# Kernel optimization log

Measured on AMD Instinct MI355X. Metric: run time of the kernel, lower is better.

## Reference

```python
import jax, jax.numpy as jnp
import numpy as np

N = 100000   # nodes
E = 1600000  # edges
D_IN = 128
H = 64
L = 3        # num SAGE layers
G = 512      # graphs in batch


def setup_inputs() -> dict:
    key = jax.random.key(0)
    ks = jax.random.split(key, 12)
    s = 0.05
    return {
        "x": jax.random.normal(ks[0], (N, D_IN), dtype=jnp.float32),
        "edge_index": jax.random.randint(ks[1], (2, E), 0, N, dtype=jnp.int64),
        "edge_attr": jax.random.normal(ks[2], (E, 1), dtype=jnp.float32),
        "batch": jnp.sort(jax.random.randint(ks[3], (N,), 0, G, dtype=jnp.int64)),
        "W0": jax.random.normal(ks[4], (D_IN, H), dtype=jnp.float32) * s,
        "b0": jnp.zeros((H,), dtype=jnp.float32),
        "Wl": jax.random.normal(ks[5], (L, H, H), dtype=jnp.float32) * s,  # lin_l (aggregated neighbors), has bias
        "bl": jnp.zeros((L, H), dtype=jnp.float32),
        "Wr": jax.random.normal(ks[6], (L, H, H), dtype=jnp.float32) * s,  # lin_r (root), no bias
        "W1": jax.random.normal(ks[7], (H, H), dtype=jnp.float32) * s,
        "b1": jnp.zeros((H,), dtype=jnp.float32),
    }


def reference(x, edge_index, edge_attr, batch, W0, b0, Wl, bl, Wr, W1, b1):
    # edge_attr is accepted but unused, matching the torch module.
    h = jax.nn.relu(x @ W0 + b0)                    # [N, H]
    src, dst = edge_index[0], edge_index[1]
    ones_e = jnp.ones((E,), dtype=h.dtype)
    deg = jax.ops.segment_sum(ones_e, dst, num_segments=N)
    deg = jnp.clip(deg, 1.0)[:, None]               # avoid div by zero (PyG mean -> 0 for isolated)
    for i in range(L):
        # SAGEConv: mean-aggregate source features onto targets, then lin_l(agg)+lin_r(h)
        agg = jax.ops.segment_sum(h[src], dst, num_segments=N) / deg  # [N, H]
        h = jax.nn.relu(agg @ Wl[i] + bl[i] + h @ Wr[i])
    # global_mean_pool over batch ids
    cnt = jax.ops.segment_sum(jnp.ones((N,), dtype=h.dtype), batch, num_segments=G)
    pooled = jax.ops.segment_sum(h, batch, num_segments=G) / jnp.clip(cnt, 1.0)[:, None]  # [G, H]
    return pooled @ W1 + b1                          # [G, H]
```

## Files before the change

### kernel.cpp

```cpp
#include <hip/hip_runtime.h>
#include <hip/hip_bf16.h>

#define NN 100000
#define NE 1600000
#define DIN 128
#define NG 512
#define MAXD 64
#define NBUK 391
#define BCAP 5120
#define CHUNK ((NE + NBUK - 1) / NBUK)
#define NTILE ((NN + 63) >> 6)

typedef __attribute__((ext_vector_type(8))) __bf16 bf16x8;
typedef __attribute__((ext_vector_type(4))) float f32x4;

static __device__ __forceinline__ unsigned short bfhi(float f) {
    __hip_bfloat16 h = __float2bfloat16(f);
    return *reinterpret_cast<unsigned short*>(&h);
}
static __device__ __forceinline__ float bf2f(unsigned short u) {
    unsigned v = (unsigned)u << 16;
    return __uint_as_float(v);
}
static __device__ __forceinline__ bf16x8 ldfrag(const void* p) {
    bf16x8 r;
    __builtin_memcpy(&r, p, 16);
    return r;
}
static __device__ __forceinline__ int swz(int a) {
    return a ^ (((a >> 8) & 3) << 5) ^ (((a >> 12) & 3) << 4);
}


#define GB 256
__global__ void __launch_bounds__(512) k_front(const int* __restrict__ src,
                                               const int* __restrict__ dst,
                                               int* __restrict__ cursor,
                                               unsigned int* __restrict__ bucket,
                                               const float* __restrict__ x,
                                               const float* __restrict__ W0,
                                               const float* __restrict__ b0,
                                               float* __restrict__ h) {
    __shared__ unsigned short sS[2 * 8192];
    __shared__ int lcnt[NBUK];
    __shared__ int lbase[NBUK];
    if (blockIdx.x < NBUK) {
        for (int i = threadIdx.x; i < NBUK; i += 512) lcnt[i] = 0;
        __syncthreads();
        int e0 = blockIdx.x * CHUNK;
        int e1 = min(e0 + CHUNK, NE);
        for (int e = e0 + (int)threadIdx.x; e < e1; e += 512)
            atomicAdd(&lcnt[dst[e] >> 8], 1);
        __syncthreads();
        for (int i = threadIdx.x; i < NBUK; i += 512) {
            int c = lcnt[i];
            lbase[i] = c ? atomicAdd(&cursor[i], c) : 0;
            lcnt[i] = 0;
        }
        __syncthreads();
        for (int e = e0 + (int)threadIdx.x; e < e1; e += 512) {
            int d = dst[e];
            int s = src[e];
            int bk = d >> 8;
            int pos = lbase[bk] + atomicAdd(&lcnt[bk], 1);
            if (pos < BCAP)
                bucket[(size_t)bk * BCAP + pos] = ((unsigned)s << 8) | (unsigned)(d & 255);
        }
    } else {
        unsigned short* sP0 = sS;
        unsigned short* sP1 = sS + 8192;
        for (int i = threadIdx.x; i < 8192; i += 512) {
            int k = i >> 6, c = i & 63;
            int slot = ((k >> 5) << 2) | (c >> 4);
            int ln   = (((k >> 3) & 3) << 4) | (c & 15);
            int ba   = swz((((((slot << 6) | ln) << 3) | (k & 7)) << 1));
            float w0 = W0[i];
            unsigned short hh = bfhi(w0);
            *(unsigned short*)((char*)sP0 + ba) = hh;
            *(unsigned short*)((char*)sP1 + ba) = bfhi(w0 - bf2f(hh));
        }
        __syncthreads();
        int lane = threadIdx.x & 63;
        int wv   = threadIdx.x >> 6;
        int cb   = wv & 3;
        int rbh  = wv >> 2;
        int col  = (cb << 4) | (lane & 15);
        float bj = b0[col];
        int r0   = (lane >> 4) << 2;
        bf16x8 Bh[4], Bl[4];
#pragma unroll
        for (int ks = 0; ks < 4; ++ks) {
            int bb = swz(((((ks << 2) | cb) << 6) | lane) << 4);
            Bh[ks] = ldfrag((const char*)sP0 + bb);
            Bl[ks] = ldfrag((const char*)sP1 + bb);
        }
        for (int t = blockIdx.x - NBUK; t < NTILE; t += GB) {
            int n0 = t << 6;
            __syncthreads();
#pragma unroll
            for (int i = 0; i < 4; ++i) {
                int tau = (int)threadIdx.x + (i << 9);
                int r = tau >> 5, kq = tau & 31;
                int n = n0 + r;
                float4 v = make_float4(0.f, 0.f, 0.f, 0.f);
                if (n < NN) v = *(const float4*)(x + ((size_t)n << 7) + (kq << 2));
                int k0   = kq << 2;
                int slot = ((k0 >> 5) << 2) | (r >> 4);
                int ln   = (((k0 >> 3) & 3) << 4) | (r & 15);
                int ba   = swz((((((slot << 6) | ln) << 3) | (k0 & 7)) << 1));
                unsigned short h0 = bfhi(v.x), h1 = bfhi(v.y),
                               h2 = bfhi(v.z), h3 = bfhi(v.w);
                *(ushort4*)((char*)sP0 + ba) = make_ushort4(h0, h1, h2, h3);
                *(ushort4*)((char*)sP1 + ba) = make_ushort4(
                    bfhi(v.x - bf2f(h0)), bfhi(v.y - bf2f(h1)),
                    bfhi(v.z - bf2f(h2)), bfhi(v.w - bf2f(h3)));
            }
            __syncthreads();
            f32x4 acc[2] = {{0.f,0.f,0.f,0.f},{0.f,0.f,0.f,0.f}};
#pragma unroll
            for (int ks = 0; ks < 4; ++ks) {
#pragma unroll
                for (int rl = 0; rl < 2; ++rl) {
                    int rb = (rbh << 1) | rl;
                    int ab = swz(((((ks << 2) | rb) << 6) | lane) << 4);
                    bf16x8 ah = ldfrag((const char*)sP0 + ab);
                    bf16x8 al = ldfrag((const char*)sP1 + ab);
                    acc[rl] = __builtin_amdgcn_mfma_f32_16x16x32_bf16(ah, Bh[ks], acc[rl], 0, 0, 0);
                    acc[rl] = __builtin_amdgcn_mfma_f32_16x16x32_bf16(ah, Bl[ks], acc[rl], 0, 0, 0);
                    acc[rl] = __builtin_amdgcn_mfma_f32_16x16x32_bf16(al, Bh[ks], acc[rl], 0, 0, 0);
                }
            }
#pragma unroll
            for (int rl = 0; rl < 2; ++rl) {
                int rb = (rbh << 1) | rl;
#pragma unroll
                for (int reg = 0; reg < 4; ++reg) {
                    int row = (rb << 4) + r0 + reg;
                    int n = n0 + row;
                    if (n < NN)
                        h[((size_t)n << 6) + col] = fmaxf(acc[rl][reg] + bj, 0.f);
                }
            }
        }
    }
}

__device__ __forceinline__ void gemmLR_mfma(unsigned short* sS,
                                            int tid, int nblk, int bidx,
                                            float* __restrict__ h_r,
                                            __hip_bfloat16* __restrict__ g,
                                            const float* __restrict__ Wl,
                                            const float* __restrict__ bl,
                                            const float* __restrict__ Wr) {
    unsigned short* sP0 = sS;
    unsigned short* sP1 = sS + 4096;
    int lane = tid & 63;
    int cb   = tid >> 6;
    bf16x8 BLh[2], BLl[2], BRh[2], BRl[2];
    for (int i = tid; i < 4096; i += 256) {
        int k = i >> 6, c = i & 63;
        int slot = ((k >> 5) << 2) | (c >> 4);
        int ln   = (((k >> 3) & 3) << 4) | (c & 15);
        int ba   = swz((((((slot << 6) | ln) << 3) | (k & 7)) << 1));
        float w = Wl[i];
        unsigned short hh = bfhi(w);
        *(unsigned short*)((char*)sP0 + ba) = hh;
        *(unsigned short*)((char*)sP1 + ba) = bfhi(w - bf2f(hh));
    }
    __syncthreads();
#pragma unroll
    for (int ks = 0; ks < 2; ++ks) {
        int bb = swz(((((ks << 2) | cb) << 6) | lane) << 4);
        BLh[ks] = ldfrag((const char*)sP0 + bb);
        BLl[ks] = ldfrag((const char*)sP1 + bb);
    }
    __syncthreads();
    for (int i = tid; i < 4096; i += 256) {
        int k = i >> 6, c = i & 63;
        int slot = ((k >> 5) << 2) | (c >> 4);
        int ln   = (((k >> 3) & 3) << 4) | (c & 15);
        int ba   = swz((((((slot << 6) | ln) << 3) | (k & 7)) << 1));
        float w = Wr[i];
        unsigned short hh = bfhi(w);
        *(unsigned short*)((char*)sP0 + ba) = hh;
        *(unsigned short*)((char*)sP1 + ba) = bfhi(w - bf2f(hh));
    }
    __syncthreads();
#pragma unroll
    for (int ks = 0; ks < 2; ++ks) {
        int bb = swz(((((ks << 2) | cb) << 6) | lane) << 4);
        BRh[ks] = ldfrag((const char*)sP0 + bb);
        BRl[ks] = ldfrag((const char*)sP1 + bb);
    }
    int col = (cb << 4) | (lane & 15);
    float bj = bl[col];
    int r0  = (lane >> 4) << 2;
    unsigned short* gp = (unsigned short*)g;
    for (int t = bidx; t < NTILE; t += nblk) {
        int n0 = t << 6;
        __syncthreads();
#pragma unroll
        for (int i = 0; i < 4; ++i) {
            int tau = tid + (i << 8);
            int r = tau >> 4, kq = tau & 15;
            int n = n0 + r;
            float4 v = make_float4(0.f, 0.f, 0.f, 0.f);
            if (n < NN) v = *(const float4*)(h_r + ((size_t)n << 6) + (kq << 2));
            int k0   = kq << 2;
            int slot = ((k0 >> 5) << 2) | (r >> 4);
            int ln   = (((k0 >> 3) & 3) << 4) | (r & 15);
            int ba   = swz((((((slot << 6) | ln) << 3) | (k0 & 7)) << 1));
            unsigned short h0 = bfhi(v.x), h1 = bfhi(v.y),
                           h2 = bfhi(v.z), h3 = bfhi(v.w);
            *(ushort4*)((char*)sP0 + ba) = make_ushort4(h0, h1, h2, h3);
            *(ushort4*)((char*)sP1 + ba) = make_ushort4(
                bfhi(v.x - bf2f(h0)), bfhi(v.y - bf2f(h1)),
                bfhi(v.z - bf2f(h2)), bfhi(v.w - bf2f(h3)));
        }
        __syncthreads();
        f32x4 accl[4] = {{0.f,0.f,0.f,0.f},{0.f,0.f,0.f,0.f},
                         {0.f,0.f,0.f,0.f},{0.f,0.f,0.f,0.f}};
        f32x4 accr[4] = {{0.f,0.f,0.f,0.f},{0.f,0.f,0.f,0.f},
                         {0.f,0.f,0.f,0.f},{0.f,0.f,0.f,0.f}};
#pragma unroll
        for (int ks = 0; ks < 2; ++ks) {
#pragma unroll
            for (int rb = 0; rb < 4; ++rb) {
                int ab = swz(((((ks << 2) | rb) << 6) | lane) << 4);
                bf16x8 ah = ldfrag((const char*)sP0 + ab);
                bf16x8 al = ldfrag((const char*)sP1 + ab);
                accl[rb] = __builtin_amdgcn_mfma_f32_16x16x32_bf16(ah, BLh[ks], accl[rb], 0, 0, 0);
                accl[rb] = __builtin_amdgcn_mfma_f32_16x16x32_bf16(ah, BLl[ks], accl[rb], 0, 0, 0);
                accl[rb] = __builtin_amdgcn_mfma_f32_16x16x32_bf16(al, BLh[ks], accl[rb], 0, 0, 0);
                accr[rb] = __builtin_amdgcn_mfma_f32_16x16x32_bf16(ah, BRh[ks], accr[rb], 0, 0, 0);
                accr[rb] = __builtin_amdgcn_mfma_f32_16x16x32_bf16(ah, BRl[ks], accr[rb], 0, 0, 0);
                accr[rb] = __builtin_amdgcn_mfma_f32_16x16x32_bf16(al, BRh[ks], accr[rb], 0, 0, 0);
            }
        }
#pragma unroll
        for (int rb = 0; rb < 4; ++rb) {
#pragma unroll
            for (int reg = 0; reg < 4; ++reg) {
                int row = (rb << 4) + r0 + reg;
                int n = n0 + row;
                if (n < NN) {
                    size_t o = ((size_t)n << 6) + col;
                    gp[o]  = bfhi(accl[rb][reg]);
                    h_r[o] = accr[rb][reg] + bj;
                }
            }
        }
    }
}

#define MGB 512
__global__ void __launch_bounds__(256) k_mid(const unsigned int* __restrict__ bucket,
                                             const int* __restrict__ cursor,
                                             int* __restrict__ cnt,
                                             int* __restrict__ ell,
                                             float* __restrict__ h_r,
                                             __hip_bfloat16* __restrict__ g,
                                             const float* __restrict__ Wl,
                                             const float* __restrict__ bl,
                                             const float* __restrict__ Wr) {
    __shared__ unsigned short sS[2 * 4096];
    __shared__ int lc[256];
    if (blockIdx.x < NBUK) {
        lc[threadIdx.x] = 0;
        int b = blockIdx.x;
        int4* ep = (int4*)(ell + (((size_t)b << 8) * MAXD));
        for (int i = threadIdx.x; i < (256 * MAXD) / 4; i += 256)
            ep[i] = make_int4(NN, NN, NN, NN);
        __syncthreads();
        int m = min(cursor[b], BCAP);
        const unsigned int* bp = bucket + (size_t)b * BCAP;
        for (int i = threadIdx.x; i < m; i += 256) {
            unsigned v = bp[i];
            int dlo = (int)(v & 255u);
            int s   = (int)(v >> 8);
            int p   = atomicAdd(&lc[dlo], 1);
            if (p < MAXD)
                ell[(((size_t)b << 8) + dlo) * MAXD + p] = s;
        }
        __syncthreads();
        int n = (b << 8) + (int)threadIdx.x;
        if (n < NN) cnt[n] = lc[threadIdx.x];
    } else {
        gemmLR_mfma(sS, threadIdx.x, MGB, blockIdx.x - NBUK, h_r, g, Wl, bl, Wr);
    }
}

__global__ void __launch_bounds__(256) k_gemmLR(float* __restrict__ h_r,
                                                __hip_bfloat16* __restrict__ g,
                                                const float* __restrict__ Wl,
                                                const float* __restrict__ bl,
                                                const float* __restrict__ Wr) {
    __shared__ unsigned short sS[2 * 4096];
    gemmLR_mfma(sS, threadIdx.x, gridDim.x, blockIdx.x, h_r, g, Wl, bl, Wr);
}

#define ACCU(U) { \
    a0 += __uint_as_float((U).x << 16); a1 += __uint_as_float((U).x & 0xffff0000u); \
    a2 += __uint_as_float((U).y << 16); a3 += __uint_as_float((U).y & 0xffff0000u); \
    a4 += __uint_as_float((U).z << 16); a5 += __uint_as_float((U).z & 0xffff0000u); \
    a6 += __uint_as_float((U).w << 16); a7 += __uint_as_float((U).w & 0xffff0000u); }
__global__ void __launch_bounds__(256) k_gather(const uint4* __restrict__ g4,
                                                float* __restrict__ r_h,
                                                const int* __restrict__ cnt,
                                                const int* __restrict__ ell) {
    int lane = threadIdx.x & 63;
    int o    = lane >> 3;
    int c8   = lane & 7;
    int wv = __builtin_amdgcn_readfirstlane((int)((blockIdx.x * 256 + threadIdx.x) >> 6));
    int nw = (gridDim.x * 256) >> 6;
    for (int p = wv; p < NN / 8; p += nw) {
        int myn = 8 * p + o;
        int d   = cnt[myn];
        int dm  = max(d, __shfl_xor(d, 8));
        dm      = max(dm, __shfl_xor(dm, 16));
        dm      = max(dm, __shfl_xor(dm, 32));
        int iters = (min(dm, MAXD) + 7) & ~7;
        const int* er = ell + ((size_t)myn << 6) + (c8 << 3);
        int4 l0 = *(const int4*)er;
        int4 l1 = *(const int4*)(er + 4);
        float a0=0.f,a1=0.f,a2=0.f,a3=0.f,a4=0.f,a5=0.f,a6=0.f,a7=0.f;
        if (iters > 0) {
            int sl = o << 3;
            uint4 c0 = g4[(size_t)__shfl(l0.x, sl) * 8 + c8];
            uint4 c1 = g4[(size_t)__shfl(l0.y, sl) * 8 + c8];
            uint4 c2 = g4[(size_t)__shfl(l0.z, sl) * 8 + c8];
            uint4 c3 = g4[(size_t)__shfl(l0.w, sl) * 8 + c8];
            uint4 c4 = g4[(size_t)__shfl(l1.x, sl) * 8 + c8];
            uint4 c5 = g4[(size_t)__shfl(l1.y, sl) * 8 + c8];
            uint4 c6 = g4[(size_t)__shfl(l1.z, sl) * 8 + c8];
            uint4 c7 = g4[(size_t)__shfl(l1.w, sl) * 8 + c8];
            for (int j0 = 8; j0 < iters; j0 += 8) {
                int s2 = (o << 3) | (j0 >> 3);
                uint4 n0v = g4[(size_t)__shfl(l0.x, s2) * 8 + c8];
                uint4 n1v = g4[(size_t)__shfl(l0.y, s2) * 8 + c8];
                uint4 n2v = g4[(size_t)__shfl(l0.z, s2) * 8 + c8];
                uint4 n3v = g4[(size_t)__shfl(l0.w, s2) * 8 + c8];
                uint4 n4v = g4[(size_t)__shfl(l1.x, s2) * 8 + c8];
                uint4 n5v = g4[(size_t)__shfl(l1.y, s2) * 8 + c8];
                uint4 n6v = g4[(size_t)__shfl(l1.z, s2) * 8 + c8];
                uint4 n7v = g4[(size_t)__shfl(l1.w, s2) * 8 + c8];
                ACCU(c0); ACCU(c1); ACCU(c2); ACCU(c3);
                ACCU(c4); ACCU(c5); ACCU(c6); ACCU(c7);
                c0 = n0v; c1 = n1v; c2 = n2v; c3 = n3v;
                c4 = n4v; c5 = n5v; c6 = n6v; c7 = n7v;
            }
            ACCU(c0); ACCU(c1); ACCU(c2); ACCU(c3);
            ACCU(c4); ACCU(c5); ACCU(c6); ACCU(c7);
        }
        float inv = 1.0f / fmaxf((float)d, 1.0f);
        float4* rp = (float4*)(r_h + ((size_t)myn << 6) + (c8 << 3));
        float4 rv0 = rp[0], rv1 = rp[1];
        rv0.x = fmaxf(fmaf(a0, inv, rv0.x), 0.0f);
        rv0.y = fmaxf(fmaf(a1, inv, rv0.y), 0.0f);
        rv0.z = fmaxf(fmaf(a2, inv, rv0.z), 0.0f);
        rv0.w = fmaxf(fmaf(a3, inv, rv0.w), 0.0f);
        rv1.x = fmaxf(fmaf(a4, inv, rv1.x), 0.0f);
        rv1.y = fmaxf(fmaf(a5, inv, rv1.y), 0.0f);
        rv1.z = fmaxf(fmaf(a6, inv, rv1.z), 0.0f);
        rv1.w = fmaxf(fmaf(a7, inv, rv1.w), 0.0f);
        rp[0] = rv0; rp[1] = rv1;
    }
}

__global__ void __launch_bounds__(256) k_pool(const int* __restrict__ batch,
                                              const float* __restrict__ h,
                                              float* __restrict__ pool,
                                              float* __restrict__ cntg) {
    int lane = threadIdx.x & 63;
    int wid  = (blockIdx.x * 256 + threadIdx.x) >> 6;
    int nw   = (gridDim.x * 256) >> 6;
    int chunk = (NN + nw - 1) / nw;
    int n0 = wid * chunk;
    if (n0 >= NN) return;
    int n1 = min(n0 + chunk, NN);
    int cur = batch[n0];
    float acc = 0.0f, acc_c = 0.0f;
    for (int n = n0; n < n1; ++n) {
        int b = batch[n];
        if (b != cur) {
            atomicAdd(&pool[(size_t)cur * 64 + lane], acc);
            if (lane == 0) atomicAdd(&cntg[cur], acc_c);
            acc = 0.0f; acc_c = 0.0f; cur = b;
        }
        acc   += h[(size_t)n * 64 + lane];
        acc_c += 1.0f;
    }
    atomicAdd(&pool[(size_t)cur * 64 + lane], acc);
    if (lane == 0) atomicAdd(&cntg[cur], acc_c);
}

__global__ void __launch_bounds__(256) k_out(const float* __restrict__ pool,
                                             const float* __restrict__ cntg,
                                             const float* __restrict__ W1,
                                             const float* __restrict__ b1,
                                             float* __restrict__ out) {
    __shared__ float sW[64 * 64];
    for (int i = threadIdx.x; i < 64 * 64; i += 256) sW[i] = W1[i];
    __syncthreads();
    int lane = threadIdx.x & 63;
    int wid  = (blockIdx.x * 256 + threadIdx.x) >> 6;
    int nw   = (gridDim.x * 256) >> 6;
    for (int gidx = wid; gidx < NG; gidx += nw) {
        float ic = 1.0f / fmaxf(cntg[gidx], 1.0f);
        float acc = 0.0f;
#pragma unroll
        for (int k = 0; k < 64; ++k)
            acc = fmaf(pool[(size_t)gidx * 64 + k], sW[k * 64 + lane], acc);
        out[(size_t)gidx * 64 + lane] = fmaf(acc, ic, b1[lane]);
    }
}

extern "C" void kernel_launch(void* const* d_in, const int* in_sizes, int n_in,
                              void* d_out, int out_size, void* d_ws, size_t ws_size,
                              hipStream_t stream) {
    const float* x     = (const float*)d_in[0];
    const int*   ei    = (const int*)d_in[1];
    const int*   batch = (const int*)d_in[3];
    const float* W0    = (const float*)d_in[4];
    const float* b0    = (const float*)d_in[5];
    const float* Wl    = (const float*)d_in[6];
    const float* bl    = (const float*)d_in[7];
    const float* Wr    = (const float*)d_in[8];
    const float* W1    = (const float*)d_in[9];
    const float* b1    = (const float*)d_in[10];
    float* out = (float*)d_out;

    char* ws = (char*)d_ws;
    size_t off = 0;
    auto alloc = [&](size_t bytes) -> void* {
        void* p = ws + off;
        off += (bytes + 255) & ~(size_t)255;
        return p;
    };
    float*          A      = (float*)alloc((size_t)NN * 64 * 4);
    __hip_bfloat16* G      = (__hip_bfloat16*)alloc((size_t)NN * 64 * 2);
    size_t zstart = off;
    (void)alloc((size_t)MAXD * 2);
    int*   cursor = (int*)alloc((size_t)NBUK * 4);
    float* pool   = (float*)alloc((size_t)NG * 64 * 4);
    float* cntg   = (float*)alloc((size_t)NG * 4);
    size_t zlen = off - zstart;
    int*          ell    = (int*)alloc((size_t)NBUK * 256 * MAXD * 4);
    unsigned int* bucket = (unsigned int*)alloc((size_t)NBUK * BCAP * 4);
    int*          cnt    = (int*)alloc((size_t)NN * 4);

    const int* src = ei;
    const int* dst = ei + NE;

    hipMemsetAsync(ws + zstart, 0, zlen, stream);

    k_front<<<NBUK + GB, 512, 0, stream>>>(src, dst, cursor, bucket, x, W0, b0, A);
    k_mid<<<NBUK + MGB, 256, 0, stream>>>(bucket, cursor, cnt, ell, A, G,
                                          Wl, bl, Wr);
    k_gather<<<3200, 256, 0, stream>>>((const uint4*)G, A, cnt, ell);

    for (int l = 1; l < 3; ++l) {
        k_gemmLR<<<512, 256, 0, stream>>>(A, G,
                                          Wl + (size_t)l * 64 * 64,
                                          bl + (size_t)l * 64,
                                          Wr + (size_t)l * 64 * 64);
        k_gather<<<3200, 256, 0, stream>>>((const uint4*)G, A, cnt, ell);
    }

    k_pool<<<256, 256, 0, stream>>>(batch, A, pool, cntg);
    k_out<<<128, 256, 0, stream>>>(pool, cntg, W1, b1, out);
}
```

Baseline: 407.6 us.

## Build ELL adjacency directly with global atomics, drop bucket pass

Replaces the two-stage bucket sort (local histogram, bucket scatter, then per-bucket ELL fill in k_mid) with a single pass that atomically increments a per-node global counter and writes the source straight into the ELL row. The k_mid kernel is removed and layer 0 now runs through the regular gemmLR kernel, so the ELL prefill with sentinel values is gone. The gather loop instead masks out-of-degree slots to the sentinel row NN per index rather than relying on prefilled padding, and loses its software-pipelined prefetch. This saves a kernel launch and a round trip through the bucket buffer, at the cost of heavy global atomic contention on random destinations and a less overlapped gather loop.

```diff
diff --git a/kernel.cpp b/kernel.cpp
--- a/kernel.cpp
+++ b/kernel.cpp
@@ -6,9 +6,6 @@
 #define DIN 128
 #define NG 512
 #define MAXD 64
-#define NBUK 391
-#define BCAP 5120
-#define CHUNK ((NE + NBUK - 1) / NBUK)
 #define NTILE ((NN + 63) >> 6)
 
 typedef __attribute__((ext_vector_type(8))) __bf16 bf16x8;
@@ -32,39 +29,38 @@
 }
 
 
+#define BB 384
 #define GB 256
 __global__ void __launch_bounds__(512) k_front(const int* __restrict__ src,
                                                const int* __restrict__ dst,
-                                               int* __restrict__ cursor,
-                                               unsigned int* __restrict__ bucket,
+                                               int* __restrict__ cnt,
+                                               int* __restrict__ ell,
                                                const float* __restrict__ x,
                                                const float* __restrict__ W0,
                                                const float* __restrict__ b0,
                                                float* __restrict__ h) {
     __shared__ unsigned short sS[2 * 8192];
-    __shared__ int lcnt[NBUK];
-    __shared__ int lbase[NBUK];
-    if (blockIdx.x < NBUK) {
-        for (int i = threadIdx.x; i < NBUK; i += 512) lcnt[i] = 0;
-        __syncthreads();
-        int e0 = blockIdx.x * CHUNK;
-        int e1 = min(e0 + CHUNK, NE);
-        for (int e = e0 + (int)threadIdx.x; e < e1; e += 512)
-            atomicAdd(&lcnt[dst[e] >> 8], 1);
-        __syncthreads();
-        for (int i = threadIdx.x; i < NBUK; i += 512) {
-            int c = lcnt[i];
-            lbase[i] = c ? atomicAdd(&cursor[i], c) : 0;
-            lcnt[i] = 0;
-        }
-        __syncthreads();
-        for (int e = e0 + (int)threadIdx.x; e < e1; e += 512) {
-            int d = dst[e];
-            int s = src[e];
-            int bk = d >> 8;
-            int pos = lbase[bk] + atomicAdd(&lcnt[bk], 1);
-            if (pos < BCAP)
-                bucket[(size_t)bk * BCAP + pos] = ((unsigned)s << 8) | (unsigned)(d & 255);
+    if (blockIdx.x < BB) {
+        const int T = BB * 512;
+        int e = blockIdx.x * 512 + (int)threadIdx.x;
+        for (; e + 3 * T < NE; e += 4 * T) {
+            int d0 = dst[e];         int s0 = src[e];
+            int d1 = dst[e + T];     int s1 = src[e + T];
+            int d2 = dst[e + 2 * T]; int s2 = src[e + 2 * T];
+            int d3 = dst[e + 3 * T]; int s3 = src[e + 3 * T];
+            int p0 = atomicAdd(&cnt[d0], 1);
+            int p1 = atomicAdd(&cnt[d1], 1);
+            int p2 = atomicAdd(&cnt[d2], 1);
+            int p3 = atomicAdd(&cnt[d3], 1);
+            if (p0 < MAXD) ell[((size_t)d0 << 6) + p0] = s0;
+            if (p1 < MAXD) ell[((size_t)d1 << 6) + p1] = s1;
+            if (p2 < MAXD) ell[((size_t)d2 << 6) + p2] = s2;
+            if (p3 < MAXD) ell[((size_t)d3 << 6) + p3] = s3;
+        }
+        for (; e < NE; e += T) {
+            int d = dst[e]; int s = src[e];
+            int p = atomicAdd(&cnt[d], 1);
+            if (p < MAXD) ell[((size_t)d << 6) + p] = s;
         }
     } else {
         unsigned short* sP0 = sS;
@@ -94,7 +90,7 @@
             Bh[ks] = ldfrag((const char*)sP0 + bb);
             Bl[ks] = ldfrag((const char*)sP1 + bb);
         }
-        for (int t = blockIdx.x - NBUK; t < NTILE; t += GB) {
+        for (int t = blockIdx.x - BB; t < NTILE; t += GB) {
             int n0 = t << 6;
             __syncthreads();
 #pragma unroll
@@ -253,43 +249,6 @@
     }
 }
 
-#define MGB 512
-__global__ void __launch_bounds__(256) k_mid(const unsigned int* __restrict__ bucket,
-                                             const int* __restrict__ cursor,
-                                             int* __restrict__ cnt,
-                                             int* __restrict__ ell,
-                                             float* __restrict__ h_r,
-                                             __hip_bfloat16* __restrict__ g,
-                                             const float* __restrict__ Wl,
-                                             const float* __restrict__ bl,
-                                             const float* __restrict__ Wr) {
-    __shared__ unsigned short sS[2 * 4096];
-    __shared__ int lc[256];
-    if (blockIdx.x < NBUK) {
-        lc[threadIdx.x] = 0;
-        int b = blockIdx.x;
-        int4* ep = (int4*)(ell + (((size_t)b << 8) * MAXD));
-        for (int i = threadIdx.x; i < (256 * MAXD) / 4; i += 256)
-            ep[i] = make_int4(NN, NN, NN, NN);
-        __syncthreads();
-        int m = min(cursor[b], BCAP);
-        const unsigned int* bp = bucket + (size_t)b * BCAP;
-        for (int i = threadIdx.x; i < m; i += 256) {
-            unsigned v = bp[i];
-            int dlo = (int)(v & 255u);
-            int s   = (int)(v >> 8);
-            int p   = atomicAdd(&lc[dlo], 1);
-            if (p < MAXD)
-                ell[(((size_t)b << 8) + dlo) * MAXD + p] = s;
-        }
-        __syncthreads();
-        int n = (b << 8) + (int)threadIdx.x;
-        if (n < NN) cnt[n] = lc[threadIdx.x];
-    } else {
-        gemmLR_mfma(sS, threadIdx.x, MGB, blockIdx.x - NBUK, h_r, g, Wl, bl, Wr);
-    }
-}
-
 __global__ void __launch_bounds__(256) k_gemmLR(float* __restrict__ h_r,
                                                 __hip_bfloat16* __restrict__ g,
                                                 const float* __restrict__ Wl,
@@ -316,41 +275,43 @@
     for (int p = wv; p < NN / 8; p += nw) {
         int myn = 8 * p + o;
         int d   = cnt[myn];
-        int dm  = max(d, __shfl_xor(d, 8));
+        int dc  = min(d, MAXD);
+        int dm  = max(dc, __shfl_xor(dc, 8));
         dm      = max(dm, __shfl_xor(dm, 16));
         dm      = max(dm, __shfl_xor(dm, 32));
-        int iters = (min(dm, MAXD) + 7) & ~7;
+        int iters = (dm + 7) & ~7;
         const int* er = ell + ((size_t)myn << 6) + (c8 << 3);
         int4 l0 = *(const int4*)er;
         int4 l1 = *(const int4*)(er + 4);
         float a0=0.f,a1=0.f,a2=0.f,a3=0.f,a4=0.f,a5=0.f,a6=0.f,a7=0.f;
-        if (iters > 0) {
-            int sl = o << 3;
-            uint4 c0 = g4[(size_t)__shfl(l0.x, sl) * 8 + c8];
-            uint4 c1 = g4[(size_t)__shfl(l0.y, sl) * 8 + c8];
-            uint4 c2 = g4[(size_t)__shfl(l0.z, sl) * 8 + c8];
-            uint4 c3 = g4[(size_t)__shfl(l0.w, sl) * 8 + c8];
-            uint4 c4 = g4[(size_t)__shfl(l1.x, sl) * 8 + c8];
-            uint4 c5 = g4[(size_t)__shfl(l1.y, sl) * 8 + c8];
-            uint4 c6 = g4[(size_t)__shfl(l1.z, sl) * 8 + c8];
-            uint4 c7 = g4[(size_t)__shfl(l1.w, sl) * 8 + c8];
-            for (int j0 = 8; j0 < iters; j0 += 8) {
-                int s2 = (o << 3) | (j0 >> 3);
-                uint4 n0v = g4[(size_t)__shfl(l0.x, s2) * 8 + c8];
-                uint4 n1v = g4[(size_t)__shfl(l0.y, s2) * 8 + c8];
-                uint4 n2v = g4[(size_t)__shfl(l0.z, s2) * 8 + c8];
-                uint4 n3v = g4[(size_t)__shfl(l0.w, s2) * 8 + c8];
-                uint4 n4v = g4[(size_t)__shfl(l1.x, s2) * 8 + c8];
-                uint4 n5v = g4[(size_t)__shfl(l1.y, s2) * 8 + c8];
-                uint4 n6v = g4[(size_t)__shfl(l1.z, s2) * 8 + c8];
-                uint4 n7v = g4[(size_t)__shfl(l1.w, s2) * 8 + c8];
-                ACCU(c0); ACCU(c1); ACCU(c2); ACCU(c3);
-                ACCU(c4); ACCU(c5); ACCU(c6); ACCU(c7);
-                c0 = n0v; c1 = n1v; c2 = n2v; c3 = n3v;
-                c4 = n4v; c5 = n5v; c6 = n6v; c7 = n7v;
-            }
-            ACCU(c0); ACCU(c1); ACCU(c2); ACCU(c3);
-            ACCU(c4); ACCU(c5); ACCU(c6); ACCU(c7);
+        for (int j0 = 0; j0 < iters; j0 += 8) {
+            int sl = (o << 3) | (j0 >> 3);
+            int i0 = __shfl(l0.x, sl);
+            int i1 = __shfl(l0.y, sl);
+            int i2 = __shfl(l0.z, sl);
+            int i3 = __shfl(l0.w, sl);
+            int i4 = __shfl(l1.x, sl);
+            int i5 = __shfl(l1.y, sl);
+            int i6 = __shfl(l1.z, sl);
+            int i7 = __shfl(l1.w, sl);
+            i0 = (j0 + 0 < d) ? i0 : NN;
+            i1 = (j0 + 1 < d) ? i1 : NN;
+            i2 = (j0 + 2 < d) ? i2 : NN;
+            i3 = (j0 + 3 < d) ? i3 : NN;
+            i4 = (j0 + 4 < d) ? i4 : NN;
+            i5 = (j0 + 5 < d) ? i5 : NN;
+            i6 = (j0 + 6 < d) ? i6 : NN;
+            i7 = (j0 + 7 < d) ? i7 : NN;
+            uint4 u0 = g4[(size_t)i0 * 8 + c8];
+            uint4 u1 = g4[(size_t)i1 * 8 + c8];
+            uint4 u2 = g4[(size_t)i2 * 8 + c8];
+            uint4 u3 = g4[(size_t)i3 * 8 + c8];
+            uint4 u4 = g4[(size_t)i4 * 8 + c8];
+            uint4 u5 = g4[(size_t)i5 * 8 + c8];
+            uint4 u6 = g4[(size_t)i6 * 8 + c8];
+            uint4 u7 = g4[(size_t)i7 * 8 + c8];
+            ACCU(u0); ACCU(u1); ACCU(u2); ACCU(u3);
+            ACCU(u4); ACCU(u5); ACCU(u6); ACCU(u7);
         }
         float inv = 1.0f / fmaxf((float)d, 1.0f);
         float4* rp = (float4*)(r_h + ((size_t)myn << 6) + (c8 << 3));
@@ -441,30 +402,25 @@
     __hip_bfloat16* G      = (__hip_bfloat16*)alloc((size_t)NN * 64 * 2);
     size_t zstart = off;
     (void)alloc((size_t)MAXD * 2);
-    int*   cursor = (int*)alloc((size_t)NBUK * 4);
+    int*   cnt    = (int*)alloc((size_t)NN * 4);
     float* pool   = (float*)alloc((size_t)NG * 64 * 4);
     float* cntg   = (float*)alloc((size_t)NG * 4);
     size_t zlen = off - zstart;
-    int*          ell    = (int*)alloc((size_t)NBUK * 256 * MAXD * 4);
-    unsigned int* bucket = (unsigned int*)alloc((size_t)NBUK * BCAP * 4);
-    int*          cnt    = (int*)alloc((size_t)NN * 4);
+    int*   ell    = (int*)alloc((size_t)NN * MAXD * 4);
 
     const int* src = ei;
     const int* dst = ei + NE;
 
     hipMemsetAsync(ws + zstart, 0, zlen, stream);
 
-    k_front<<<NBUK + GB, 512, 0, stream>>>(src, dst, cursor, bucket, x, W0, b0, A);
-    k_mid<<<NBUK + MGB, 256, 0, stream>>>(bucket, cursor, cnt, ell, A, G,
-                                          Wl, bl, Wr);
-    k_gather<<<3200, 256, 0, stream>>>((const uint4*)G, A, cnt, ell);
-
-    for (int l = 1; l < 3; ++l) {
+    k_front<<<BB + GB, 512, 0, stream>>>(src, dst, cnt, ell, x, W0, b0, A);
+
+    for (int l = 0; l < 3; ++l) {
         k_gemmLR<<<512, 256, 0, stream>>>(A, G,
                                           Wl + (size_t)l * 64 * 64,
                                           bl + (size_t)l * 64,
                                           Wr + (size_t)l * 64 * 64);
-        k_gather<<<3200, 256, 0, stream>>>((const uint4*)G, A, cnt, ell);
+        k_gather<<<3125, 256, 0, stream>>>((const uint4*)G, A, cnt, ell);
     }
 
     k_pool<<<256, 256, 0, stream>>>(batch, A, pool, cntg);
```

After: 486.7 us. 19.4% more time.

## Fuse neighbor gather with next layer's GEMM into one kernel

Applied to the files above, without the earlier changes.

Adds a k_gg kernel that performs the mean-aggregation gather for a tile of 64 nodes, then immediately computes the next layer's lin_l and lin_r products with split-bf16 MFMA from LDS. This replaces the separate gather and gemmLR launches for the middle layers, and ping-pongs the bf16 feature buffer so the fused kernel does not race on its own input. ELL sentinel initialization is dropped. Padding lanes are now masked by degree to point at a zeroed sentinel row, which saves a large fill but adds per-edge selects. It also removes the software prefetch in the gather loop, which may expose more memory latency.

```diff
diff --git a/kernel.cpp b/kernel.cpp
--- a/kernel.cpp
+++ b/kernel.cpp
@@ -268,9 +268,6 @@
     if (blockIdx.x < NBUK) {
         lc[threadIdx.x] = 0;
         int b = blockIdx.x;
-        int4* ep = (int4*)(ell + (((size_t)b << 8) * MAXD));
-        for (int i = threadIdx.x; i < (256 * MAXD) / 4; i += 256)
-            ep[i] = make_int4(NN, NN, NN, NN);
         __syncthreads();
         int m = min(cursor[b], BCAP);
         const unsigned int* bp = bucket + (size_t)b * BCAP;
@@ -290,20 +287,180 @@
     }
 }
 
-__global__ void __launch_bounds__(256) k_gemmLR(float* __restrict__ h_r,
-                                                __hip_bfloat16* __restrict__ g,
-                                                const float* __restrict__ Wl,
-                                                const float* __restrict__ bl,
-                                                const float* __restrict__ Wr) {
-    __shared__ unsigned short sS[2 * 4096];
-    gemmLR_mfma(sS, threadIdx.x, gridDim.x, blockIdx.x, h_r, g, Wl, bl, Wr);
-}
-
 #define ACCU(U) { \
     a0 += __uint_as_float((U).x << 16); a1 += __uint_as_float((U).x & 0xffff0000u); \
     a2 += __uint_as_float((U).y << 16); a3 += __uint_as_float((U).y & 0xffff0000u); \
     a4 += __uint_as_float((U).z << 16); a5 += __uint_as_float((U).z & 0xffff0000u); \
     a6 += __uint_as_float((U).w << 16); a7 += __uint_as_float((U).w & 0xffff0000u); }
+
+#define FB 512
+__global__ void __launch_bounds__(512) k_gg(const uint4* __restrict__ gin,
+                                            float* __restrict__ rA,
+                                            unsigned short* __restrict__ gout,
+                                            const int* __restrict__ cnt,
+                                            const int* __restrict__ ell,
+                                            const float* __restrict__ Wl,
+                                            const float* __restrict__ bl,
+                                            const float* __restrict__ Wr) {
+    __shared__ unsigned short sS[2 * 4096];
+    unsigned short* sP0 = sS;
+    unsigned short* sP1 = sS + 4096;
+    int tid = (int)threadIdx.x;
+    int lane = tid & 63;
+    int w    = tid >> 6;
+    int cb   = w & 3;
+    int rbh  = w >> 2;
+    bf16x8 BLh[2], BLl[2], BRh[2], BRl[2];
+    for (int i = tid; i < 4096; i += 512) {
+        int k = i >> 6, c = i & 63;
+        int slot = ((k >> 5) << 2) | (c >> 4);
+        int ln   = (((k >> 3) & 3) << 4) | (c & 15);
+        int ba   = swz((((((slot << 6) | ln) << 3) | (k & 7)) << 1));
+        float wv_ = Wl[i];
+        unsigned short hh = bfhi(wv_);
+        *(unsigned short*)((char*)sP0 + ba) = hh;
+        *(unsigned short*)((char*)sP1 + ba) = bfhi(wv_ - bf2f(hh));
+    }
+    __syncthreads();
+#pragma unroll
+    for (int ks = 0; ks < 2; ++ks) {
+        int bb = swz(((((ks << 2) | cb) << 6) | lane) << 4);
+        BLh[ks] = ldfrag((const char*)sP0 + bb);
+        BLl[ks] = ldfrag((const char*)sP1 + bb);
+    }
+    __syncthreads();
+    for (int i = tid; i < 4096; i += 512) {
+        int k = i >> 6, c = i & 63;
+        int slot = ((k >> 5) << 2) | (c >> 4);
+        int ln   = (((k >> 3) & 3) << 4) | (c & 15);
+        int ba   = swz((((((slot << 6) | ln) << 3) | (k & 7)) << 1));
+        float wv_ = Wr[i];
+        unsigned short hh = bfhi(wv_);
+        *(unsigned short*)((char*)sP0 + ba) = hh;
+        *(unsigned short*)((char*)sP1 + ba) = bfhi(wv_ - bf2f(hh));
+    }
+    __syncthreads();
+#pragma unroll
+    for (int ks = 0; ks < 2; ++ks) {
+        int bb = swz(((((ks << 2) | cb) << 6) | lane) << 4);
+        BRh[ks] = ldfrag((const char*)sP0 + bb);
+        BRl[ks] = ldfrag((const char*)sP1 + bb);
+    }
+    int col = (cb << 4) | (lane & 15);
+    float bj = bl[col];
+    int r0  = (lane >> 4) << 2;
+    int o   = lane >> 3;
+    int c8  = lane & 7;
+    for (int t = blockIdx.x; t < NTILE; t += FB) {
+        int n0t = t << 6;
+        int myn = n0t + (w << 3) + o;
+        int d = (myn < NN) ? cnt[myn] : 0;
+        int dc = min(d, MAXD);
+        int dm = max(dc, __shfl_xor(dc, 8));
+        dm     = max(dm, __shfl_xor(dm, 16));
+        dm     = max(dm, __shfl_xor(dm, 32));
+        int iters = (dm + 7) & ~7;
+        const int* er = ell + ((size_t)min(myn, NN - 1) << 6) + (c8 << 3);
+        int4 l0 = *(const int4*)er;
+        int4 l1 = *(const int4*)(er + 4);
+        float a0=0.f,a1=0.f,a2=0.f,a3=0.f,a4=0.f,a5=0.f,a6=0.f,a7=0.f;
+        for (int j0 = 0; j0 < iters; j0 += 8) {
+            int sl = (o << 3) | (j0 >> 3);
+            int i0 = __shfl(l0.x, sl);
+            int i1 = __shfl(l0.y, sl);
+            int i2 = __shfl(l0.z, sl);
+            int i3 = __shfl(l0.w, sl);
+            int i4 = __shfl(l1.x, sl);
+            int i5 = __shfl(l1.y, sl);
+            int i6 = __shfl(l1.z, sl);
+            int i7 = __shfl(l1.w, sl);
+            i0 = (j0 + 0 < d) ? i0 : NN;
+            i1 = (j0 + 1 < d) ? i1 : NN;
+            i2 = (j0 + 2 < d) ? i2 : NN;
+            i3 = (j0 + 3 < d) ? i3 : NN;
+            i4 = (j0 + 4 < d) ? i4 : NN;
+            i5 = (j0 + 5 < d) ? i5 : NN;
+            i6 = (j0 + 6 < d) ? i6 : NN;
+            i7 = (j0 + 7 < d) ? i7 : NN;
+            uint4 u0 = gin[(size_t)i0 * 8 + c8];
+            uint4 u1 = gin[(size_t)i1 * 8 + c8];
+            uint4 u2 = gin[(size_t)i2 * 8 + c8];
+            uint4 u3 = gin[(size_t)i3 * 8 + c8];
+            uint4 u4 = gin[(size_t)i4 * 8 + c8];
+            uint4 u5 = gin[(size_t)i5 * 8 + c8];
+            uint4 u6 = gin[(size_t)i6 * 8 + c8];
+            uint4 u7 = gin[(size_t)i7 * 8 + c8];
+            ACCU(u0); ACCU(u1); ACCU(u2); ACCU(u3);
+            ACCU(u4); ACCU(u5); ACCU(u6); ACCU(u7);
+        }
+        float4 rv0 = make_float4(0.f,0.f,0.f,0.f), rv1 = rv0;
+        if (myn < NN) {
+            float inv = 1.0f / fmaxf((float)d, 1.0f);
+            const float4* rp = (const float4*)(rA + ((size_t)myn << 6) + (c8 << 3));
+            rv0 = rp[0]; rv1 = rp[1];
+            rv0.x = fmaxf(fmaf(a0, inv, rv0.x), 0.0f);
+            rv0.y = fmaxf(fmaf(a1, inv, rv0.y), 0.0f);
+            rv0.z = fmaxf(fmaf(a2, inv, rv0.z), 0.0f);
+            rv0.w = fmaxf(fmaf(a3, inv, rv0.w), 0.0f);
+            rv1.x = fmaxf(fmaf(a4, inv, rv1.x), 0.0f);
+            rv1.y = fmaxf(fmaf(a5, inv, rv1.y), 0.0f);
+            rv1.z = fmaxf(fmaf(a6, inv, rv1.z), 0.0f);
+            rv1.w = fmaxf(fmaf(a7, inv, rv1.w), 0.0f);
+        }
+        __syncthreads();
+        {
+            int rr = (w << 3) + o;
+#pragma unroll
+            for (int half = 0; half < 2; ++half) {
+                float4 v = half ? rv1 : rv0;
+                int k0 = (c8 << 3) + (half << 2);
+                int slot = ((k0 >> 5) << 2) | (rr >> 4);
+                int ln   = (((k0 >> 3) & 3) << 4) | (rr & 15);
+                int ba   = swz((((((slot << 6) | ln) << 3) | (k0 & 7)) << 1));
+                unsigned short h0 = bfhi(v.x), h1 = bfhi(v.y),
+                               h2 = bfhi(v.z), h3 = bfhi(v.w);
+                *(ushort4*)((char*)sP0 + ba) = make_ushort4(h0, h1, h2, h3);
+                *(ushort4*)((char*)sP1 + ba) = make_ushort4(
+                    bfhi(v.x - bf2f(h0)), bfhi(v.y - bf2f(h1)),
+                    bfhi(v.z - bf2f(h2)), bfhi(v.w - bf2f(h3)));
+            }
+        }
+        __syncthreads();
+        f32x4 accl[2] = {{0.f,0.f,0.f,0.f},{0.f,0.f,0.f,0.f}};
+        f32x4 accr[2] = {{0.f,0.f,0.f,0.f},{0.f,0.f,0.f,0.f}};
+#pragma unroll
+        for (int ks = 0; ks < 2; ++ks) {
+#pragma unroll
+            for (int rl = 0; rl < 2; ++rl) {
+                int rb = (rbh << 1) | rl;
+                int ab = swz(((((ks << 2) | rb) << 6) | lane) << 4);
+                bf16x8 ah = ldfrag((const char*)sP0 + ab);
+                bf16x8 al = ldfrag((const char*)sP1 + ab);
+                accl[rl] = __builtin_amdgcn_mfma_f32_16x16x32_bf16(ah, BLh[ks], accl[rl], 0, 0, 0);
+                accl[rl] = __builtin_amdgcn_mfma_f32_16x16x32_bf16(ah, BLl[ks], accl[rl], 0, 0, 0);
+                accl[rl] = __builtin_amdgcn_mfma_f32_16x16x32_bf16(al, BLh[ks], accl[rl], 0, 0, 0);
+                accr[rl] = __builtin_amdgcn_mfma_f32_16x16x32_bf16(ah, BRh[ks], accr[rl], 0, 0, 0);
+                accr[rl] = __builtin_amdgcn_mfma_f32_16x16x32_bf16(ah, BRl[ks], accr[rl], 0, 0, 0);
+                accr[rl] = __builtin_amdgcn_mfma_f32_16x16x32_bf16(al, BRh[ks], accr[rl], 0, 0, 0);
+            }
+        }
+#pragma unroll
+        for (int rl = 0; rl < 2; ++rl) {
+            int rb = (rbh << 1) | rl;
+#pragma unroll
+            for (int reg = 0; reg < 4; ++reg) {
+                int row = (rb << 4) + r0 + reg;
+                int n = n0t + row;
+                if (n < NN) {
+                    size_t off = ((size_t)n << 6) + col;
+                    gout[off] = bfhi(accl[rl][reg]);
+                    rA[off]   = accr[rl][reg] + bj;
+                }
+            }
+        }
+    }
+}
+
 __global__ void __launch_bounds__(256) k_gather(const uint4* __restrict__ g4,
                                                 float* __restrict__ r_h,
                                                 const int* __restrict__ cnt,
@@ -316,41 +473,43 @@
     for (int p = wv; p < NN / 8; p += nw) {
         int myn = 8 * p + o;
         int d   = cnt[myn];
-        int dm  = max(d, __shfl_xor(d, 8));
+        int dc  = min(d, MAXD);
+        int dm  = max(dc, __shfl_xor(dc, 8));
         dm      = max(dm, __shfl_xor(dm, 16));
         dm      = max(dm, __shfl_xor(dm, 32));
-        int iters = (min(dm, MAXD) + 7) & ~7;
+        int iters = (dm + 7) & ~7;
         const int* er = ell + ((size_t)myn << 6) + (c8 << 3);
         int4 l0 = *(const int4*)er;
         int4 l1 = *(const int4*)(er + 4);
         float a0=0.f,a1=0.f,a2=0.f,a3=0.f,a4=0.f,a5=0.f,a6=0.f,a7=0.f;
-        if (iters > 0) {
-            int sl = o << 3;
-            uint4 c0 = g4[(size_t)__shfl(l0.x, sl) * 8 + c8];
-            uint4 c1 = g4[(size_t)__shfl(l0.y, sl) * 8 + c8];
-            uint4 c2 = g4[(size_t)__shfl(l0.z, sl) * 8 + c8];
-            uint4 c3 = g4[(size_t)__shfl(l0.w, sl) * 8 + c8];
-            uint4 c4 = g4[(size_t)__shfl(l1.x, sl) * 8 + c8];
-            uint4 c5 = g4[(size_t)__shfl(l1.y, sl) * 8 + c8];
-            uint4 c6 = g4[(size_t)__shfl(l1.z, sl) * 8 + c8];
-            uint4 c7 = g4[(size_t)__shfl(l1.w, sl) * 8 + c8];
-            for (int j0 = 8; j0 < iters; j0 += 8) {
-                int s2 = (o << 3) | (j0 >> 3);
-                uint4 n0v = g4[(size_t)__shfl(l0.x, s2) * 8 + c8];
-                uint4 n1v = g4[(size_t)__shfl(l0.y, s2) * 8 + c8];
-                uint4 n2v = g4[(size_t)__shfl(l0.z, s2) * 8 + c8];
-                uint4 n3v = g4[(size_t)__shfl(l0.w, s2) * 8 + c8];
-                uint4 n4v = g4[(size_t)__shfl(l1.x, s2) * 8 + c8];
-                uint4 n5v = g4[(size_t)__shfl(l1.y, s2) * 8 + c8];
-                uint4 n6v = g4[(size_t)__shfl(l1.z, s2) * 8 + c8];
-                uint4 n7v = g4[(size_t)__shfl(l1.w, s2) * 8 + c8];
-                ACCU(c0); ACCU(c1); ACCU(c2); ACCU(c3);
-                ACCU(c4); ACCU(c5); ACCU(c6); ACCU(c7);
-                c0 = n0v; c1 = n1v; c2 = n2v; c3 = n3v;
-                c4 = n4v; c5 = n5v; c6 = n6v; c7 = n7v;
-            }
-            ACCU(c0); ACCU(c1); ACCU(c2); ACCU(c3);
-            ACCU(c4); ACCU(c5); ACCU(c6); ACCU(c7);
+        for (int j0 = 0; j0 < iters; j0 += 8) {
+            int sl = (o << 3) | (j0 >> 3);
+            int i0 = __shfl(l0.x, sl);
+            int i1 = __shfl(l0.y, sl);
+            int i2 = __shfl(l0.z, sl);
+            int i3 = __shfl(l0.w, sl);
+            int i4 = __shfl(l1.x, sl);
+            int i5 = __shfl(l1.y, sl);
+            int i6 = __shfl(l1.z, sl);
+            int i7 = __shfl(l1.w, sl);
+            i0 = (j0 + 0 < d) ? i0 : NN;
+            i1 = (j0 + 1 < d) ? i1 : NN;
+            i2 = (j0 + 2 < d) ? i2 : NN;
+            i3 = (j0 + 3 < d) ? i3 : NN;
+            i4 = (j0 + 4 < d) ? i4 : NN;
+            i5 = (j0 + 5 < d) ? i5 : NN;
+            i6 = (j0 + 6 < d) ? i6 : NN;
+            i7 = (j0 + 7 < d) ? i7 : NN;
+            uint4 u0 = g4[(size_t)i0 * 8 + c8];
+            uint4 u1 = g4[(size_t)i1 * 8 + c8];
+            uint4 u2 = g4[(size_t)i2 * 8 + c8];
+            uint4 u3 = g4[(size_t)i3 * 8 + c8];
+            uint4 u4 = g4[(size_t)i4 * 8 + c8];
+            uint4 u5 = g4[(size_t)i5 * 8 + c8];
+            uint4 u6 = g4[(size_t)i6 * 8 + c8];
+            uint4 u7 = g4[(size_t)i7 * 8 + c8];
+            ACCU(u0); ACCU(u1); ACCU(u2); ACCU(u3);
+            ACCU(u4); ACCU(u5); ACCU(u6); ACCU(u7);
         }
         float inv = 1.0f / fmaxf((float)d, 1.0f);
         float4* rp = (float4*)(r_h + ((size_t)myn << 6) + (c8 << 3));
@@ -437,35 +596,35 @@
         off += (bytes + 255) & ~(size_t)255;
         return p;
     };
-    float*          A      = (float*)alloc((size_t)NN * 64 * 4);
-    __hip_bfloat16* G      = (__hip_bfloat16*)alloc((size_t)NN * 64 * 2);
-    size_t zstart = off;
-    (void)alloc((size_t)MAXD * 2);
+    float*          A  = (float*)alloc((size_t)NN * 64 * 4);
+    unsigned short* G0 = (unsigned short*)alloc((size_t)NN * 128);
+    size_t z1start = off;
+    (void)alloc(256);
+    unsigned short* G1 = (unsigned short*)alloc((size_t)NN * 128);
+    size_t z2start = off;
+    (void)alloc(256);
     int*   cursor = (int*)alloc((size_t)NBUK * 4);
     float* pool   = (float*)alloc((size_t)NG * 64 * 4);
     float* cntg   = (float*)alloc((size_t)NG * 4);
-    size_t zlen = off - zstart;
-    int*          ell    = (int*)alloc((size_t)NBUK * 256 * MAXD * 4);
+    size_t z2len = off - z2start;
+    int*          ell    = (int*)alloc((size_t)NN * MAXD * 4);
     unsigned int* bucket = (unsigned int*)alloc((size_t)NBUK * BCAP * 4);
     int*          cnt    = (int*)alloc((size_t)NN * 4);
 
     const int* src = ei;
     const int* dst = ei + NE;
 
-    hipMemsetAsync(ws + zstart, 0, zlen, stream);
+    hipMemsetAsync(ws + z1start, 0, 256, stream);
+    hipMemsetAsync(ws + z2start, 0, z2len, stream);
 
     k_front<<<NBUK + GB, 512, 0, stream>>>(src, dst, cursor, bucket, x, W0, b0, A);
-    k_mid<<<NBUK + MGB, 256, 0, stream>>>(bucket, cursor, cnt, ell, A, G,
-                                          Wl, bl, Wr);
-    k_gather<<<3200, 256, 0, stream>>>((const uint4*)G, A, cnt, ell);
-
-    for (int l = 1; l < 3; ++l) {
-        k_gemmLR<<<512, 256, 0, stream>>>(A, G,
-                                          Wl + (size_t)l * 64 * 64,
-                                          bl + (size_t)l * 64,
-                                          Wr + (size_t)l * 64 * 64);
-        k_gather<<<3200, 256, 0, stream>>>((const uint4*)G, A, cnt, ell);
-    }
+    k_mid<<<NBUK + MGB, 256, 0, stream>>>(bucket, cursor, cnt, ell, A,
+                                          (__hip_bfloat16*)G0, Wl, bl, Wr);
+    k_gg<<<FB, 512, 0, stream>>>((const uint4*)G0, A, G1, cnt, ell,
+                                 Wl + (size_t)1 * 64 * 64, bl + 64, Wr + (size_t)1 * 64 * 64);
+    k_gg<<<FB, 512, 0, stream>>>((const uint4*)G1, A, G0, cnt, ell,
+                                 Wl + (size_t)2 * 64 * 64, bl + 128, Wr + (size_t)2 * 64 * 64);
+    k_gather<<<3125, 256, 0, stream>>>((const uint4*)G0, A, cnt, ell);
 
     k_pool<<<256, 256, 0, stream>>>(batch, A, pool, cntg);
     k_out<<<128, 256, 0, stream>>>(pool, cntg, W1, b1, out);
```

New measurement: 377.7 us. -7.4%, faster.
